# Kernel optimization log

Measured on AMD Instinct MI355X. Metric: run time of the kernel, lower is better.

The kernel has to match this reference:

```python
import jax
import jax.numpy as jnp
from jax import lax
import numpy as np

B, T, C = 64, 512, 256
EPS = 1e-8
INF = jnp.float32(1e9)


def setup_inputs() -> dict:
    key = jax.random.key(0)
    x = jax.random.normal(key, (B, T, C), dtype=jnp.float32)
    return {"x": x, "num_clusters": 8}


def _cluster_single(x, num_clusters):
    # x: [T, C]. Average-linkage agglomerative clustering with cosine distance.
    t = x.shape[0]
    xn = x / (jnp.linalg.norm(x, axis=-1, keepdims=True) + EPS)
    d = 1.0 - xn @ xn.T                      # [T, T] cosine distance
    eye = jnp.eye(t, dtype=bool)
    d = jnp.where(eye, INF, d)
    sizes = jnp.ones((t,), dtype=jnp.float32)
    assign = jnp.arange(t, dtype=jnp.int32)  # cluster representative per token

    n_merges = t - num_clusters              # static Python int

    def body(_, state):
        d, sizes, assign = state
        flat = jnp.argmin(d)
        i0, j0 = flat // t, flat % t
        i = jnp.minimum(i0, j0).astype(jnp.int32)
        j = jnp.maximum(i0, j0).astype(jnp.int32)
        ni, nj = sizes[i], sizes[j]
        # average linkage: size-weighted mean of the two merged rows
        newrow = (ni * d[i] + nj * d[j]) / (ni + nj)
        d = d.at[i].set(newrow).at[:, i].set(newrow)
        d = d.at[i, i].set(INF)
        d = d.at[j].set(INF).at[:, j].set(INF)
        sizes = sizes.at[i].add(nj).at[j].set(0.0)
        assign = jnp.where(assign == j, i, assign)
        return d, sizes, assign

    d, sizes, assign = lax.fori_loop(0, n_merges, body, (d, sizes, assign))

    # canonical relabel: clusters numbered 0..k-1 by first token occurrence
    eq = assign[:, None] == assign[None, :]          # [T, T]
    first = jnp.argmax(eq, axis=1)                   # first index of each cluster
    is_first = jnp.arange(t) == first
    ranks = jnp.cumsum(is_first.astype(jnp.int32)) - 1
    return ranks[first]                              # [T] int32 labels


def reference(x, num_clusters):
    k = min(int(num_clusters), x.shape[1])  # num_clusters = min(num_clusters, T)
    labels = jax.vmap(lambda xb: _cluster_single(xb, k))(x)  # [B, T]
    return labels
```

## Files before the change

kernel.cpp:

```cpp
#include <hip/hip_runtime.h>
#include <hip/hip_bf16.h>

#pragma clang fp contract(off)

#define TT 512
#define CC 256
#define TPAD 257
#define INFV 1e9f

__device__ __forceinline__ unsigned long long packkey(float v, unsigned c) {
  return ((unsigned long long)__float_as_uint(v) << 32) | (unsigned long long)c;
}

__device__ __forceinline__ unsigned long long wave_min_u64(unsigned long long k) {
#pragma unroll
  for (int off = 32; off >= 1; off >>= 1) {
    unsigned long long o = __shfl_xor(k, off, 64);
    if (o < k) k = o;
  }
  return k;
}

__device__ void load_norm_tile(const float* __restrict__ xb, int rowBase,
                               float (*S)[TPAD], double* part, int tid) {
  for (int idx = tid; idx < 64 * CC; idx += 256) {
    int r = idx >> 8;
    int c = idx & (CC - 1);
    S[r][c] = xb[(size_t)(rowBase + r) * CC + c];
  }
  __syncthreads();
  {
    int r = tid >> 2, p = tid & 3;
    double s = 0.0;
    int c0 = p * 64;
    for (int c = 0; c < 64; ++c) {
      double v = (double)S[r][c0 + c];
      s = fma(v, v, s);
    }
    part[tid] = s;
  }
  __syncthreads();
  if ((tid & 3) == 0) {
    double tot = part[tid] + part[tid + 1] + part[tid + 2] + part[tid + 3];
    part[tid] = sqrt(tot) + 1e-8;
  }
  __syncthreads();
  for (int idx = tid; idx < 64 * CC; idx += 256) {
    int r = idx >> 8;
    int c = idx & (CC - 1);
    S[r][c] = (float)((double)S[r][c] / part[r << 2]);
  }
  __syncthreads();
}

__global__ __launch_bounds__(256) void build_dist_kernel(
    const float* __restrict__ x, float* __restrict__ dall,
    unsigned long long* __restrict__ rkall) {
  __shared__ float A[64][TPAD];
  __shared__ float Bs[64][TPAD];
  __shared__ double part[256];
  __shared__ unsigned long long rkl[64];

  int ta = blockIdx.x;
  int b  = blockIdx.y;
  const float* xb = x + (size_t)b * TT * CC;
  float* d = dall + (size_t)b * TT * TT;
  int tid = threadIdx.x;
  if (tid < 64) rkl[tid] = ~0ull;
  load_norm_tile(xb, ta * 64, A, part, tid);

  int ty = tid & 15;
  int tx = tid >> 4;
  for (int tb = 0; tb < 8; ++tb) {
    __syncthreads();
    load_norm_tile(xb, tb * 64, Bs, part, tid);
    double acc[4][4];
#pragma unroll
    for (int ia = 0; ia < 4; ++ia)
#pragma unroll
      for (int ib = 0; ib < 4; ++ib) acc[ia][ib] = 0.0;
    for (int k = 0; k < CC; ++k) {
      double av[4], bv[4];
#pragma unroll
      for (int ia = 0; ia < 4; ++ia) av[ia] = (double)A[4 * tx + ia][k];
#pragma unroll
      for (int ib = 0; ib < 4; ++ib) bv[ib] = (double)Bs[4 * ty + ib][k];
#pragma unroll
      for (int ia = 0; ia < 4; ++ia)
#pragma unroll
        for (int ib = 0; ib < 4; ++ib)
          acc[ia][ib] = fma(av[ia], bv[ib], acc[ia][ib]);
    }
#pragma unroll
    for (int ia = 0; ia < 4; ++ia) {
      int gr = ta * 64 + 4 * tx + ia;
      int gcBase = tb * 64 + 4 * ty;
      float vt[4];
      unsigned long long key = ~0ull;
#pragma unroll
      for (int ib = 0; ib < 4; ++ib) {
        int gc = gcBase + ib;
        float v = (gr == gc) ? INFV : (float)(1.0 - acc[ia][ib]);
        vt[ib] = v;
        unsigned long long kk = packkey(v, (unsigned)gc);
        if (kk < key) key = kk;
      }
      *(float4*)(&d[(size_t)gr * TT + gcBase]) =
          make_float4(vt[0], vt[1], vt[2], vt[3]);
#pragma unroll
      for (int off = 1; off < 16; off <<= 1) {
        unsigned long long o = __shfl_xor(key, off, 64);
        if (o < key) key = o;
      }
      if (ty == 0) atomicMin(&rkl[4 * tx + ia], key);
    }
  }
  __syncthreads();
  if (tid < 64) rkall[(size_t)b * TT + ta * 64 + tid] = rkl[tid];
}

__global__ __launch_bounds__(256) void agglom_kernel(
    const int* __restrict__ ncp, float* __restrict__ dall,
    const unsigned long long* __restrict__ rkall, int* __restrict__ outp) {
  __shared__ unsigned long long rk[TT];
  __shared__ float sizes[TT];
  __shared__ float nvs[TT];
  __shared__ int assign[TT];
  __shared__ int rankArr[TT];
  __shared__ int rlist[TT];
  __shared__ unsigned long long pm[4];
  __shared__ unsigned long long pmi[4];
  __shared__ int wsum[4];
  __shared__ int nresc;

  int b = blockIdx.x;
  int tid = threadIdx.x;
  int lane = tid & 63;
  int w = tid >> 6;
  float* d = dall + (size_t)b * TT * TT;
  int rA = tid * 2, rB = tid * 2 + 1;

  rk[rA] = rkall[(size_t)b * TT + rA];
  rk[rB] = rkall[(size_t)b * TT + rB];
  sizes[rA] = 1.0f; sizes[rB] = 1.0f;
  assign[rA] = rA;  assign[rB] = rB;
  if (tid == 0) nresc = 0;
  int K = ncp[0];
  if (K > TT) K = TT;
  if (K < 1) K = 1;
  int nm = TT - K;
  __syncthreads();

  for (int iter = 0; iter < nm; ++iter) {
    unsigned long long kA =
        (rk[rA] & 0xFFFFFFFF00000000ull) | (unsigned long long)(unsigned)rA;
    unsigned long long kB =
        (rk[rB] & 0xFFFFFFFF00000000ull) | (unsigned long long)(unsigned)rB;
    unsigned long long best = kA < kB ? kA : kB;
    best = wave_min_u64(best);
    if (lane == 0) pm[w] = best;
    __syncthreads();
    best = pm[0];
    if (pm[1] < best) best = pm[1];
    if (pm[2] < best) best = pm[2];
    if (pm[3] < best) best = pm[3];
    int i = (int)(best & 0xFFFFFFFFull);
    int j = (int)(rk[i] & 0xFFFFFFFFull);
    float ni = sizes[i], nj = sizes[j];
    float denom = ni + nj;
    if (tid == 0) nresc = 0;

    float2 a2 = *(const float2*)(d + (size_t)i * TT + rA);
    float2 b2 = *(const float2*)(d + (size_t)j * TT + rA);
    float v0 = (ni * a2.x + nj * b2.x) / denom;
    float v1 = (ni * a2.y + nj * b2.y) / denom;
    float w0 = (rA == i || rA == j) ? INFV : v0;
    float w1 = (rB == i || rB == j) ? INFV : v1;
    nvs[rA] = w0; nvs[rB] = w1;
    unsigned long long ik = packkey(w0, (unsigned)rA);
    unsigned long long ik2 = packkey(w1, (unsigned)rB);
    if (ik2 < ik) ik = ik2;
    ik = wave_min_u64(ik);
    if (lane == 0) pmi[w] = ik;
    __syncthreads();

    *(float2*)(d + (size_t)i * TT + rA) = make_float2(w0, w1);
    d[(size_t)rA * TT + i] = w0;
    d[(size_t)rB * TT + i] = w1;
    d[(size_t)rA * TT + j] = INFV;
    d[(size_t)rB * TT + j] = INFV;
    if (tid == 0) {
      unsigned long long ikey = pmi[0];
      if (pmi[1] < ikey) ikey = pmi[1];
      if (pmi[2] < ikey) ikey = pmi[2];
      if (pmi[3] < ikey) ikey = pmi[3];
      sizes[i] = denom;
      sizes[j] = 0.0f;
      rk[i] = ikey;
      rk[j] = packkey(INFV, 0xFFFFFFFFu);
    }
#pragma unroll
    for (int t = 0; t < 2; ++t) {
      int r = rA + t;
      if (r != i && r != j && sizes[r] > 0.0f) {
        unsigned long long cur = rk[r];
        unsigned c = (unsigned)(cur & 0xFFFFFFFFull);
        if (c == (unsigned)i || c == (unsigned)j) {
          int p = atomicAdd(&nresc, 1);
          rlist[p] = r;
        } else {
          unsigned long long nk = packkey(nvs[r], (unsigned)i);
          if (nk < cur) rk[r] = nk;
        }
      }
      if (assign[r] == j) assign[r] = i;
    }
    __syncthreads();

    int nr = nresc;
    for (int q = w; q < nr; q += 4) {
      int rr = rlist[q];
      const float4* p = (const float4*)(d + (size_t)rr * TT);
      float4 x0 = p[lane * 2];
      float4 x1 = p[lane * 2 + 1];
      int cb = lane * 8;
      unsigned long long key = packkey(x0.x, cb);
      unsigned long long kk;
      kk = packkey(x0.y, cb + 1); if (kk < key) key = kk;
      kk = packkey(x0.z, cb + 2); if (kk < key) key = kk;
      kk = packkey(x0.w, cb + 3); if (kk < key) key = kk;
      kk = packkey(x1.x, cb + 4); if (kk < key) key = kk;
      kk = packkey(x1.y, cb + 5); if (kk < key) key = kk;
      kk = packkey(x1.z, cb + 6); if (kk < key) key = kk;
      kk = packkey(x1.w, cb + 7); if (kk < key) key = kk;
      key = wave_min_u64(key);
      if (lane == 0) rk[rr] = key;
    }
    __syncthreads();
  }

  int f0 = (assign[rA] == rA) ? 1 : 0;
  int f1 = (assign[rB] == rB) ? 1 : 0;
  int c = f0 + f1;
  int incl = c;
#pragma unroll
  for (int off = 1; off < 64; off <<= 1) {
    int o = __shfl_up(incl, (unsigned)off, 64);
    if (lane >= off) incl += o;
  }
  if (lane == 63) wsum[w] = incl;
  __syncthreads();
  int base = incl - c;
  for (int q = 0; q < w; ++q) base += wsum[q];
  if (f0) rankArr[rA] = base;
  if (f1) rankArr[rB] = base + f0;
  __syncthreads();
  outp[(size_t)b * TT + rA] = rankArr[assign[rA]];
  outp[(size_t)b * TT + rB] = rankArr[assign[rB]];
}

extern "C" void kernel_launch(void* const* d_in, const int* in_sizes, int n_in,
                              void* d_out, int out_size, void* d_ws, size_t ws_size,
                              hipStream_t stream) {
  const float* x = (const float*)d_in[0];
  const int* ncp = (const int*)d_in[1];
  int B = in_sizes[0] / (TT * CC);
  float* dall = (float*)d_ws;
  unsigned long long* rkall =
      (unsigned long long*)((char*)d_ws + (size_t)B * TT * TT * sizeof(float));
  int* outp = (int*)d_out;

  dim3 g1(TT / 64, B);
  build_dist_kernel<<<g1, 256, 0, stream>>>(x, dall, rkall);
  agglom_kernel<<<B, 256, 0, stream>>>(ncp, dall, rkall, outp);
}
```

Before: 1.884 ms.

## Rescan invalidated rows per wave with early prefetch and fewer barriers

```diff
diff --git a/kernel.cpp b/kernel.cpp
--- a/kernel.cpp
+++ b/kernel.cpp
@@ -127,40 +127,41 @@
   __shared__ float nvs[TT];
   __shared__ int assign[TT];
   __shared__ int rankArr[TT];
-  __shared__ int rlist[TT];
   __shared__ unsigned long long pm[4];
   __shared__ unsigned long long pmi[4];
   __shared__ int wsum[4];
-  __shared__ int nresc;
 
   int b = blockIdx.x;
   int tid = threadIdx.x;
   int lane = tid & 63;
   int w = tid >> 6;
+  int wb = w * 128;
   float* d = dall + (size_t)b * TT * TT;
-  int rA = tid * 2, rB = tid * 2 + 1;
+  int rA = tid * 2, rB = rA + 1;
 
   rk[rA] = rkall[(size_t)b * TT + rA];
   rk[rB] = rkall[(size_t)b * TT + rB];
   sizes[rA] = 1.0f; sizes[rB] = 1.0f;
   assign[rA] = rA;  assign[rB] = rB;
-  if (tid == 0) nresc = 0;
   int K = ncp[0];
   if (K > TT) K = TT;
   if (K < 1) K = 1;
   int nm = TT - K;
   __syncthreads();
 
-  for (int iter = 0; iter < nm; ++iter) {
+  {
     unsigned long long kA =
         (rk[rA] & 0xFFFFFFFF00000000ull) | (unsigned long long)(unsigned)rA;
     unsigned long long kB =
         (rk[rB] & 0xFFFFFFFF00000000ull) | (unsigned long long)(unsigned)rB;
-    unsigned long long best = kA < kB ? kA : kB;
-    best = wave_min_u64(best);
-    if (lane == 0) pm[w] = best;
-    __syncthreads();
-    best = pm[0];
+    unsigned long long bst = kA < kB ? kA : kB;
+    bst = wave_min_u64(bst);
+    if (lane == 0) pm[w] = bst;
+  }
+  __syncthreads();
+
+  for (int iter = 0; iter < nm; ++iter) {
+    unsigned long long best = pm[0];
     if (pm[1] < best) best = pm[1];
     if (pm[2] < best) best = pm[2];
     if (pm[3] < best) best = pm[3];
@@ -168,10 +169,39 @@
     int j = (int)(rk[i] & 0xFFFFFFFFull);
     float ni = sizes[i], nj = sizes[j];
     float denom = ni + nj;
-    if (tid == 0) nresc = 0;
 
     float2 a2 = *(const float2*)(d + (size_t)i * TT + rA);
     float2 b2 = *(const float2*)(d + (size_t)j * TT + rA);
+
+    unsigned fl = 0;
+    {
+      if (rA != i && rA != j && sizes[rA] > 0.0f) {
+        unsigned c = (unsigned)(rk[rA] & 0xFFFFFFFFull);
+        if (c == (unsigned)i || c == (unsigned)j) fl |= 1u;
+      }
+      if (rB != i && rB != j && sizes[rB] > 0.0f) {
+        unsigned c = (unsigned)(rk[rB] & 0xFFFFFFFFull);
+        if (c == (unsigned)i || c == (unsigned)j) fl |= 2u;
+      }
+    }
+    unsigned long long mm0 = __ballot(fl & 1u);
+    unsigned long long mm1 = __ballot(fl & 2u);
+
+    int er0 = -1, er1 = -1;
+    float4 pa0, pb0, pa1, pb1;
+    if (mm0) { int l = __ffsll(mm0) - 1; mm0 &= mm0 - 1; er0 = wb + 2 * l; }
+    else if (mm1) { int l = __ffsll(mm1) - 1; mm1 &= mm1 - 1; er0 = wb + 2 * l + 1; }
+    if (er0 >= 0) {
+      const float4* p = (const float4*)(d + (size_t)er0 * TT);
+      pa0 = p[lane * 2]; pb0 = p[lane * 2 + 1];
+    }
+    if (mm0) { int l = __ffsll(mm0) - 1; mm0 &= mm0 - 1; er1 = wb + 2 * l; }
+    else if (mm1) { int l = __ffsll(mm1) - 1; mm1 &= mm1 - 1; er1 = wb + 2 * l + 1; }
+    if (er1 >= 0) {
+      const float4* p = (const float4*)(d + (size_t)er1 * TT);
+      pa1 = p[lane * 2]; pb1 = p[lane * 2 + 1];
+    }
+
     float v0 = (ni * a2.x + nj * b2.x) / denom;
     float v1 = (ni * a2.y + nj * b2.y) / denom;
     float w0 = (rA == i || rA == j) ? INFV : v0;
@@ -189,52 +219,87 @@
     d[(size_t)rB * TT + i] = w1;
     d[(size_t)rA * TT + j] = INFV;
     d[(size_t)rB * TT + j] = INFV;
-    if (tid == 0) {
+
+    if (tid == (i >> 1)) {
       unsigned long long ikey = pmi[0];
       if (pmi[1] < ikey) ikey = pmi[1];
       if (pmi[2] < ikey) ikey = pmi[2];
       if (pmi[3] < ikey) ikey = pmi[3];
+      rk[i] = ikey;
       sizes[i] = denom;
+    }
+    if (tid == (j >> 1)) {
+      rk[j] = packkey(INFV, 0xFFFFFFFFu);
       sizes[j] = 0.0f;
-      rk[i] = ikey;
-      rk[j] = packkey(INFV, 0xFFFFFFFFu);
-    }
+    }
+
 #pragma unroll
     for (int t = 0; t < 2; ++t) {
       int r = rA + t;
-      if (r != i && r != j && sizes[r] > 0.0f) {
+      if (!((fl >> t) & 1u) && r != i && r != j && sizes[r] > 0.0f) {
         unsigned long long cur = rk[r];
-        unsigned c = (unsigned)(cur & 0xFFFFFFFFull);
-        if (c == (unsigned)i || c == (unsigned)j) {
-          int p = atomicAdd(&nresc, 1);
-          rlist[p] = r;
-        } else {
-          unsigned long long nk = packkey(nvs[r], (unsigned)i);
-          if (nk < cur) rk[r] = nk;
+        unsigned long long nk = packkey(nvs[r], (unsigned)i);
+        if (nk < cur) rk[r] = nk;
+      }
+      if (assign[r] == j) assign[r] = i;
+    }
+
+    {
+      int cb = lane * 8;
+      if (er0 >= 0) {
+        float pv = nvs[er0];
+        unsigned long long key = ~0ull, kk;
+#pragma unroll
+        for (int t = 0; t < 8; ++t) {
+          int c = cb + t;
+          float e = t < 4 ? (&pa0.x)[t] : (&pb0.x)[t - 4];
+          e = (c == i) ? pv : ((c == j) ? INFV : e);
+          kk = packkey(e, (unsigned)c); if (kk < key) key = kk;
         }
-      }
-      if (assign[r] == j) assign[r] = i;
-    }
-    __syncthreads();
-
-    int nr = nresc;
-    for (int q = w; q < nr; q += 4) {
-      int rr = rlist[q];
-      const float4* p = (const float4*)(d + (size_t)rr * TT);
-      float4 x0 = p[lane * 2];
-      float4 x1 = p[lane * 2 + 1];
-      int cb = lane * 8;
-      unsigned long long key = packkey(x0.x, cb);
-      unsigned long long kk;
-      kk = packkey(x0.y, cb + 1); if (kk < key) key = kk;
-      kk = packkey(x0.z, cb + 2); if (kk < key) key = kk;
-      kk = packkey(x0.w, cb + 3); if (kk < key) key = kk;
-      kk = packkey(x1.x, cb + 4); if (kk < key) key = kk;
-      kk = packkey(x1.y, cb + 5); if (kk < key) key = kk;
-      kk = packkey(x1.z, cb + 6); if (kk < key) key = kk;
-      kk = packkey(x1.w, cb + 7); if (kk < key) key = kk;
-      key = wave_min_u64(key);
-      if (lane == 0) rk[rr] = key;
+        key = wave_min_u64(key);
+        if (lane == 0) rk[er0] = key;
+      }
+      if (er1 >= 0) {
+        float pv = nvs[er1];
+        unsigned long long key = ~0ull, kk;
+#pragma unroll
+        for (int t = 0; t < 8; ++t) {
+          int c = cb + t;
+          float e = t < 4 ? (&pa1.x)[t] : (&pb1.x)[t - 4];
+          e = (c == i) ? pv : ((c == j) ? INFV : e);
+          kk = packkey(e, (unsigned)c); if (kk < key) key = kk;
+        }
+        key = wave_min_u64(key);
+        if (lane == 0) rk[er1] = key;
+      }
+      while (mm0 | mm1) {
+        int rr;
+        if (mm0) { int l = __ffsll(mm0) - 1; mm0 &= mm0 - 1; rr = wb + 2 * l; }
+        else     { int l = __ffsll(mm1) - 1; mm1 &= mm1 - 1; rr = wb + 2 * l + 1; }
+        const float4* p = (const float4*)(d + (size_t)rr * TT);
+        float4 x0 = p[lane * 2], x1 = p[lane * 2 + 1];
+        float pv = nvs[rr];
+        unsigned long long key = ~0ull, kk;
+#pragma unroll
+        for (int t = 0; t < 8; ++t) {
+          int c = cb + t;
+          float e = t < 4 ? (&x0.x)[t] : (&x1.x)[t - 4];
+          e = (c == i) ? pv : ((c == j) ? INFV : e);
+          kk = packkey(e, (unsigned)c); if (kk < key) key = kk;
+        }
+        key = wave_min_u64(key);
+        if (lane == 0) rk[rr] = key;
+      }
+    }
+
+    {
+      unsigned long long kA =
+          (rk[rA] & 0xFFFFFFFF00000000ull) | (unsigned long long)(unsigned)rA;
+      unsigned long long kB =
+          (rk[rB] & 0xFFFFFFFF00000000ull) | (unsigned long long)(unsigned)rB;
+      unsigned long long bst = kA < kB ? kA : kB;
+      bst = wave_min_u64(bst);
+      if (lane == 0) pm[w] = bst;
     }
     __syncthreads();
   }
```

New measurement: 2.010 ms. +6.7%, slower.

## Prefetch rescan rows early and replace column-j writes with alive bitmask

Applied to the files above, without the earlier changes.

```diff
diff --git a/kernel.cpp b/kernel.cpp
--- a/kernel.cpp
+++ b/kernel.cpp
@@ -127,24 +127,26 @@
   __shared__ float nvs[TT];
   __shared__ int assign[TT];
   __shared__ int rankArr[TT];
-  __shared__ int rlist[TT];
+  __shared__ int rlist[2][TT];
+  __shared__ unsigned aliveM[TT / 32];
   __shared__ unsigned long long pm[4];
   __shared__ unsigned long long pmi[4];
   __shared__ int wsum[4];
-  __shared__ int nresc;
+  __shared__ int nresc[2];
 
   int b = blockIdx.x;
   int tid = threadIdx.x;
   int lane = tid & 63;
   int w = tid >> 6;
   float* d = dall + (size_t)b * TT * TT;
-  int rA = tid * 2, rB = tid * 2 + 1;
+  int rA = tid * 2, rB = rA + 1;
 
   rk[rA] = rkall[(size_t)b * TT + rA];
   rk[rB] = rkall[(size_t)b * TT + rB];
   sizes[rA] = 1.0f; sizes[rB] = 1.0f;
   assign[rA] = rA;  assign[rB] = rB;
-  if (tid == 0) nresc = 0;
+  if (tid < TT / 32) aliveM[tid] = 0xFFFFFFFFu;
+  if (tid < 2) nresc[tid] = 0;
   int K = ncp[0];
   if (K > TT) K = TT;
   if (K < 1) K = 1;
@@ -152,6 +154,7 @@
   __syncthreads();
 
   for (int iter = 0; iter < nm; ++iter) {
+    int buf = iter & 1;
     unsigned long long kA =
         (rk[rA] & 0xFFFFFFFF00000000ull) | (unsigned long long)(unsigned)rA;
     unsigned long long kB =
@@ -159,6 +162,7 @@
     unsigned long long best = kA < kB ? kA : kB;
     best = wave_min_u64(best);
     if (lane == 0) pm[w] = best;
+    if (tid == 0) nresc[buf ^ 1] = 0;
     __syncthreads();
     best = pm[0];
     if (pm[1] < best) best = pm[1];
@@ -168,14 +172,30 @@
     int j = (int)(rk[i] & 0xFFFFFFFFull);
     float ni = sizes[i], nj = sizes[j];
     float denom = ni + nj;
-    if (tid == 0) nresc = 0;
 
     float2 a2 = *(const float2*)(d + (size_t)i * TT + rA);
     float2 b2 = *(const float2*)(d + (size_t)j * TT + rA);
+
+    unsigned fl = 0;
+    if (rA != i && rA != j && sizes[rA] > 0.0f) {
+      unsigned c = (unsigned)(rk[rA] & 0xFFFFFFFFull);
+      if (c == (unsigned)i || c == (unsigned)j) fl |= 1u;
+    }
+    if (rB != i && rB != j && sizes[rB] > 0.0f) {
+      unsigned c = (unsigned)(rk[rB] & 0xFFFFFFFFull);
+      if (c == (unsigned)i || c == (unsigned)j) fl |= 2u;
+    }
+    if (fl & 1u) { int p = atomicAdd(&nresc[buf], 1); rlist[buf][p] = rA; }
+    if (fl & 2u) { int p = atomicAdd(&nresc[buf], 1); rlist[buf][p] = rB; }
+
+    unsigned aw = aliveM[rA >> 5];
+    bool alA = (aw >> (rA & 31)) & 1u;
+    bool alB = (aw >> (rB & 31)) & 1u;
+
     float v0 = (ni * a2.x + nj * b2.x) / denom;
     float v1 = (ni * a2.y + nj * b2.y) / denom;
-    float w0 = (rA == i || rA == j) ? INFV : v0;
-    float w1 = (rB == i || rB == j) ? INFV : v1;
+    float w0 = (rA == i || rA == j || !alA) ? INFV : v0;
+    float w1 = (rB == i || rB == j || !alB) ? INFV : v1;
     nvs[rA] = w0; nvs[rB] = w1;
     unsigned long long ik = packkey(w0, (unsigned)rA);
     unsigned long long ik2 = packkey(w1, (unsigned)rB);
@@ -184,11 +204,22 @@
     if (lane == 0) pmi[w] = ik;
     __syncthreads();
 
+    int nr = nresc[buf];
+    int er0 = (2 * w < nr) ? rlist[buf][2 * w] : -1;
+    int er1 = (2 * w + 1 < nr) ? rlist[buf][2 * w + 1] : -1;
+    float4 pa0, pb0, pa1, pb1;
+    if (er0 >= 0) {
+      const float4* p = (const float4*)(d + (size_t)er0 * TT);
+      pa0 = p[lane * 2]; pb0 = p[lane * 2 + 1];
+    }
+    if (er1 >= 0) {
+      const float4* p = (const float4*)(d + (size_t)er1 * TT);
+      pa1 = p[lane * 2]; pb1 = p[lane * 2 + 1];
+    }
+
     *(float2*)(d + (size_t)i * TT + rA) = make_float2(w0, w1);
     d[(size_t)rA * TT + i] = w0;
     d[(size_t)rB * TT + i] = w1;
-    d[(size_t)rA * TT + j] = INFV;
-    d[(size_t)rB * TT + j] = INFV;
     if (tid == 0) {
       unsigned long long ikey = pmi[0];
       if (pmi[1] < ikey) ikey = pmi[1];
@@ -198,44 +229,45 @@
       sizes[j] = 0.0f;
       rk[i] = ikey;
       rk[j] = packkey(INFV, 0xFFFFFFFFu);
+      aliveM[j >> 5] &= ~(1u << (j & 31));
     }
 #pragma unroll
     for (int t = 0; t < 2; ++t) {
       int r = rA + t;
-      if (r != i && r != j && sizes[r] > 0.0f) {
+      if (!((fl >> t) & 1u) && r != i && r != j && sizes[r] > 0.0f) {
         unsigned long long cur = rk[r];
-        unsigned c = (unsigned)(cur & 0xFFFFFFFFull);
-        if (c == (unsigned)i || c == (unsigned)j) {
-          int p = atomicAdd(&nresc, 1);
-          rlist[p] = r;
-        } else {
-          unsigned long long nk = packkey(nvs[r], (unsigned)i);
-          if (nk < cur) rk[r] = nk;
-        }
+        unsigned long long nk = packkey(nvs[r], (unsigned)i);
+        if (nk < cur) rk[r] = nk;
       }
       if (assign[r] == j) assign[r] = i;
     }
     __syncthreads();
 
-    int nr = nresc;
-    for (int q = w; q < nr; q += 4) {
-      int rr = rlist[q];
+    int cb = lane * 8;
+    unsigned aw2 = aliveM[lane >> 2];
+#define PATCH_FOLD(RR, V0, V1)                                                \
+    {                                                                         \
+      float pv = nvs[RR];                                                     \
+      unsigned long long key = ~0ull, kk;                                     \
+      _Pragma("unroll") for (int t = 0; t < 8; ++t) {                         \
+        int c = cb + t;                                                       \
+        bool alive = (aw2 >> (((lane & 3) << 3) + t)) & 1u;                   \
+        float e = t < 4 ? (&V0.x)[t] : (&V1.x)[t - 4];                        \
+        e = (c == i) ? pv : ((c == j || !alive) ? INFV : e);                  \
+        kk = packkey(e, (unsigned)c); if (kk < key) key = kk;                 \
+      }                                                                       \
+      key = wave_min_u64(key);                                                \
+      if (lane == 0) rk[RR] = key;                                            \
+    }
+    if (er0 >= 0) PATCH_FOLD(er0, pa0, pb0);
+    if (er1 >= 0) PATCH_FOLD(er1, pa1, pb1);
+    for (int q = 8 + w; q < nr; q += 4) {
+      int rr = rlist[buf][q];
       const float4* p = (const float4*)(d + (size_t)rr * TT);
-      float4 x0 = p[lane * 2];
-      float4 x1 = p[lane * 2 + 1];
-      int cb = lane * 8;
-      unsigned long long key = packkey(x0.x, cb);
-      unsigned long long kk;
-      kk = packkey(x0.y, cb + 1); if (kk < key) key = kk;
-      kk = packkey(x0.z, cb + 2); if (kk < key) key = kk;
-      kk = packkey(x0.w, cb + 3); if (kk < key) key = kk;
-      kk = packkey(x1.x, cb + 4); if (kk < key) key = kk;
-      kk = packkey(x1.y, cb + 5); if (kk < key) key = kk;
-      kk = packkey(x1.z, cb + 6); if (kk < key) key = kk;
-      kk = packkey(x1.w, cb + 7); if (kk < key) key = kk;
-      key = wave_min_u64(key);
-      if (lane == 0) rk[rr] = key;
-    }
+      float4 x0 = p[lane * 2], x1 = p[lane * 2 + 1];
+      PATCH_FOLD(rr, x0, x1);
+    }
+#undef PATCH_FOLD
     __syncthreads();
   }
 
```

Result: slower. 2.047 ms (+8.6%).
